# Performance work log

Measured on AMD Instinct MI355X. Metric: run time of the kernel, lower is better.

The kernel has to match this reference:

```python
import jax, jax.numpy as jnp
import numpy as np

E = 1024      # d_model
H = 16        # num heads
D = E // H    # head dim = 64
FF = 4096     # dim_feedforward
WIN = 128
EPS = 1e-5    # layer-norm eps
NEG = -1e9


def setup_inputs() -> dict:
    key = jax.random.key(0)
    ks = jax.random.split(key, 16)
    s = 0.02
    f32 = jnp.float32
    return {
        "src":       jax.random.normal(ks[0], (2, 2048, E), f32),
        "in_proj_w": jax.random.normal(ks[1], (3 * E, E), f32) * s,
        "in_proj_b": jnp.zeros((3 * E,), f32),
        "out_w":     jax.random.normal(ks[2], (E, E), f32) * s,
        "out_b":     jnp.zeros((E,), f32),
        "lin1_w":    jax.random.normal(ks[3], (FF, E), f32) * s,
        "lin1_b":    jnp.zeros((FF,), f32),
        "lin2_w":    jax.random.normal(ks[4], (E, FF), f32) * s,
        "lin2_b":    jnp.zeros((E,), f32),
        "ln1_g":     jnp.ones((E,), f32),
        "ln1_beta":  jnp.zeros((E,), f32),
        "ln2_g":     jnp.ones((E,), f32),
        "ln2_beta":  jnp.zeros((E,), f32),
    }


def _layer_norm(x, g, b):
    mu = x.mean(-1, keepdims=True)
    var = ((x - mu) ** 2).mean(-1, keepdims=True)
    return (x - mu) * jax.lax.rsqrt(var + EPS) * g + b


def reference(src, in_proj_w, in_proj_b, out_w, out_b,
              lin1_w, lin1_b, lin2_w, lin2_b,
              ln1_g, ln1_beta, ln2_g, ln2_beta):
    B, L, _ = src.shape  # batch_first=True
    x = src

    # fused QKV projection (torch Linear: y = x @ W.T + b)
    qkv = x @ in_proj_w.T + in_proj_b            # [B, L, 3E]
    q, k, v = jnp.split(qkv, 3, axis=-1)
    q = q.reshape(B, L, H, D)
    k = k.reshape(B, L, H, D)
    v = v.reshape(B, L, H, D)

    scores = jnp.einsum('blhd,bmhd->bhlm', q, k) / np.float32(np.sqrt(D))
    idx = jnp.arange(L)
    band = jnp.abs(idx[:, None] - idx[None, :]) <= WIN   # [L, L] allowed positions
    scores = jnp.where(band, scores, NEG)
    attn = jax.nn.softmax(scores, axis=-1)

    ctx = jnp.einsum('bhlm,bmhd->blhd', attn, v).reshape(B, L, E)
    attn_out = ctx @ out_w.T + out_b

    # post-norm transformer encoder layer (norm_first=False default)
    x = _layer_norm(x + attn_out, ln1_g, ln1_beta)
    ff = jax.nn.relu(x @ lin1_w.T + lin1_b) @ lin2_w.T + lin2_b
    return _layer_norm(x + ff, ln2_g, ln2_beta)
```

## Files before the change

### kernel.cpp

```cpp
#include <hip/hip_runtime.h>
#include <cstdint>
#include <cstddef>


typedef __attribute__((ext_vector_type(8))) short short8;
typedef __attribute__((ext_vector_type(4))) float f32x4;

__device__ __forceinline__ float b2f(unsigned short u) {
  union { unsigned int i; float f; } x; x.i = ((unsigned int)u) << 16; return x.f;
}
__device__ __forceinline__ unsigned short f2b(float f) {
  union { float f; unsigned int i; } x; x.f = f;
  unsigned int i = x.i;
  unsigned int r = (i + 0x7FFFu + ((i >> 16) & 1u)) >> 16;
  return (unsigned short)r;
}
__device__ __forceinline__ uint4 pack8(float4 f0, float4 f1) {
  uint4 r;
  r.x = (unsigned)f2b(f0.x) | ((unsigned)f2b(f0.y) << 16);
  r.y = (unsigned)f2b(f0.z) | ((unsigned)f2b(f0.w) << 16);
  r.z = (unsigned)f2b(f1.x) | ((unsigned)f2b(f1.y) << 16);
  r.w = (unsigned)f2b(f1.z) | ((unsigned)f2b(f1.w) << 16);
  return r;
}

__device__ __forceinline__ void gl_lds16(const unsigned short* g, unsigned short* l) {
  __builtin_amdgcn_global_load_lds(
      (const __attribute__((address_space(1))) unsigned int*)g,
      (__attribute__((address_space(3))) unsigned int*)l, 16, 0, 0);
}

__global__ __launch_bounds__(256) void conv3_k(
    const float* __restrict__ src, unsigned short* __restrict__ srcb,
    const float* __restrict__ w_in, const float* __restrict__ w_out,
    unsigned short* __restrict__ wslot)
{
  const int i = (blockIdx.x * 256 + threadIdx.x) * 8;
  const float* in;
  unsigned short* out;
  if (i < 4194304)      { in = src + i;                 out = srcb + i; }
  else if (i < 7340032) { in = w_in + (i - 4194304);    out = wslot + (i - 4194304); }
  else                  { in = w_out + (i - 7340032);   out = wslot + (i - 4194304); }
  const float4 f0 = *(const float4*)(in);
  const float4 f1 = *(const float4*)(in + 4);
  *(uint4*)(out) = pack8(f0, f1);
}

__global__ __launch_bounds__(256) void conv2_k(
    const float* __restrict__ w1, unsigned short* __restrict__ o1,
    const float* __restrict__ w2, unsigned short* __restrict__ o2)
{
  const int i = (blockIdx.x * 256 + threadIdx.x) * 8;
  const float* in;
  unsigned short* out;
  if (i < 4194304) { in = w1 + i;             out = o1 + i; }
  else             { in = w2 + (i - 4194304); out = o2 + (i - 4194304); }
  const float4 f0 = *(const float4*)(in);
  const float4 f1 = *(const float4*)(in + 4);
  *(uint4*)(out) = pack8(f0, f1);
}

template<int RELU, int OUT32>
__global__ __launch_bounds__(512, 2) void gemm256(
    const unsigned short* __restrict__ A, const unsigned short* __restrict__ Wb,
    const float* __restrict__ bias, void* __restrict__ out,
    int M, int N, int K)
{
  __shared__ unsigned short As[2][256 * 64];
  __shared__ unsigned short Bs[2][256 * 64];

  const int tid = threadIdx.x;
  const int lane = tid & 63, wid = tid >> 6;
  const int wm = wid >> 2, wn = wid & 3;

  const int gx = gridDim.x;
  const int flat = blockIdx.y * gx + blockIdx.x;
  const int chunk = (gx * gridDim.y) >> 3;
  const int nf = (flat & 7) * chunk + (flat >> 3);
  const int m0 = (nf / gx) * 256, n0 = (nf % gx) * 256;

  int offA[2][2], offB[2][2], ldsO2[2][2];
#pragma unroll
  for (int h1 = 0; h1 < 2; ++h1)
#pragma unroll
    for (int i = 0; i < 2; ++i) {
      const int sl = i * 512 + tid;
      const int r = h1 * 128 + (sl >> 3);
      const int sslot = sl & 7;
      const int c = (sslot + r) & 7;
      offA[h1][i] = (m0 + r) * K + c * 8;
      offB[h1][i] = (n0 + r) * K + c * 8;
      ldsO2[h1][i] = (h1 * 1024 + i * 512 + (tid & ~63)) * 8;
    }

  const int cl = lane & 15;
  const int kg = lane >> 4;

  int aoff[4][2], boff[2][2];
#pragma unroll
  for (int mt = 0; mt < 4; ++mt) {
    const int ar = wm * 64 + mt * 16 + cl;
#pragma unroll
    for (int ks = 0; ks < 2; ++ks)
      aoff[mt][ks] = ar * 64 + (((ks * 4 + kg) - ar) & 7) * 8;
  }
#pragma unroll
  for (int nt = 0; nt < 2; ++nt) {
    const int br = wn * 32 + nt * 16 + cl;
#pragma unroll
    for (int ks = 0; ks < 2; ++ks)
      boff[nt][ks] = br * 64 + (((ks * 4 + kg) - br) & 7) * 8;
  }

  f32x4 acc[8][4];
#pragma unroll
  for (int i = 0; i < 8; ++i)
#pragma unroll
    for (int j = 0; j < 4; ++j) acc[i][j] = (f32x4){0.f, 0.f, 0.f, 0.f};

  const int steps = K >> 6;

#define STAGE256(idx_) do { const int _x = (idx_); if (_x < 4 * steps) {        \
    const int T_ = _x >> 2, j_ = _x & 3, bf_ = T_ & 1; const int ko = T_ << 6;  \
    if (j_ == 0)      { gl_lds16(A  + offA[0][0] + ko, &As[bf_][ldsO2[0][0]]);  \
                        gl_lds16(A  + offA[0][1] + ko, &As[bf_][ldsO2[0][1]]); }\
    else if (j_ == 1) { gl_lds16(Wb + offB[0][0] + ko, &Bs[bf_][ldsO2[0][0]]);  \
                        gl_lds16(Wb + offB[0][1] + ko, &Bs[bf_][ldsO2[0][1]]); }\
    else if (j_ == 2) { gl_lds16(Wb + offB[1][0] + ko, &Bs[bf_][ldsO2[1][0]]);  \
                        gl_lds16(Wb + offB[1][1] + ko, &Bs[bf_][ldsO2[1][1]]); }\
    else              { gl_lds16(A  + offA[1][0] + ko, &As[bf_][ldsO2[1][0]]);  \
                        gl_lds16(A  + offA[1][1] + ko, &As[bf_][ldsO2[1][1]]); }\
  } } while (0)

  STAGE256(0); STAGE256(1); STAGE256(2); STAGE256(3);
  STAGE256(4); STAGE256(5); STAGE256(6);
  asm volatile("s_waitcnt vmcnt(6)" ::: "memory");
  __builtin_amdgcn_s_barrier();

  int cur = 0;
  for (int s = 0; s < steps; ++s) {
    short8 bf0[2][2], af[4][2];
#pragma unroll
    for (int nt = 0; nt < 2; ++nt)
#pragma unroll
      for (int ks = 0; ks < 2; ++ks) bf0[nt][ks] = *(const short8*)&Bs[cur][boff[nt][ks]];
#pragma unroll
    for (int mt = 0; mt < 4; ++mt)
#pragma unroll
      for (int ks = 0; ks < 2; ++ks) af[mt][ks] = *(const short8*)&As[cur][aoff[mt][ks]];
    STAGE256(4 * s + 7);
    asm volatile("s_waitcnt lgkmcnt(8)" ::: "memory");
    __builtin_amdgcn_s_barrier();
    asm volatile("s_waitcnt lgkmcnt(0)" ::: "memory");
    __builtin_amdgcn_sched_barrier(0);
    __builtin_amdgcn_s_setprio(1);
#pragma unroll
    for (int mt = 0; mt < 4; ++mt)
#pragma unroll
      for (int nt = 0; nt < 2; ++nt)
#pragma unroll
        for (int ks = 0; ks < 2; ++ks)
          acc[mt][nt] = __builtin_amdgcn_mfma_f32_16x16x32_bf16(af[mt][ks], bf0[nt][ks], acc[mt][nt], 0, 0, 0);
    __builtin_amdgcn_s_setprio(0);
    __builtin_amdgcn_s_barrier();

    short8 bf1[2][2];
#pragma unroll
    for (int nt = 0; nt < 2; ++nt)
#pragma unroll
      for (int ks = 0; ks < 2; ++ks) bf1[nt][ks] = *(const short8*)&Bs[cur][boff[nt][ks] + 8192];
    STAGE256(4 * s + 8);
    __builtin_amdgcn_s_barrier();
    asm volatile("s_waitcnt lgkmcnt(0)" ::: "memory");
    __builtin_amdgcn_sched_barrier(0);
    __builtin_amdgcn_s_setprio(1);
#pragma unroll
    for (int mt = 0; mt < 4; ++mt)
#pragma unroll
      for (int nt = 0; nt < 2; ++nt)
#pragma unroll
        for (int ks = 0; ks < 2; ++ks)
          acc[mt][nt + 2] = __builtin_amdgcn_mfma_f32_16x16x32_bf16(af[mt][ks], bf1[nt][ks], acc[mt][nt + 2], 0, 0, 0);
    __builtin_amdgcn_s_setprio(0);
    __builtin_amdgcn_s_barrier();

    short8 ag[4][2];
#pragma unroll
    for (int mt = 0; mt < 4; ++mt)
#pragma unroll
      for (int ks = 0; ks < 2; ++ks) ag[mt][ks] = *(const short8*)&As[cur][aoff[mt][ks] + 8192];
    STAGE256(4 * s + 9);
    __builtin_amdgcn_s_barrier();
    asm volatile("s_waitcnt lgkmcnt(0)" ::: "memory");
    __builtin_amdgcn_sched_barrier(0);
    __builtin_amdgcn_s_setprio(1);
#pragma unroll
    for (int mt = 0; mt < 4; ++mt)
#pragma unroll
      for (int nt = 0; nt < 2; ++nt)
#pragma unroll
        for (int ks = 0; ks < 2; ++ks)
          acc[mt + 4][nt] = __builtin_amdgcn_mfma_f32_16x16x32_bf16(ag[mt][ks], bf0[nt][ks], acc[mt + 4][nt], 0, 0, 0);
    __builtin_amdgcn_s_setprio(0);
    __builtin_amdgcn_s_barrier();

    STAGE256(4 * s + 10);
    if (s < steps - 2)       asm volatile("s_waitcnt vmcnt(6)" ::: "memory");
    else if (s == steps - 2) asm volatile("s_waitcnt vmcnt(0)" ::: "memory");
    __builtin_amdgcn_s_barrier();
    __builtin_amdgcn_s_setprio(1);
#pragma unroll
    for (int mt = 0; mt < 4; ++mt)
#pragma unroll
      for (int nt = 0; nt < 2; ++nt)
#pragma unroll
        for (int ks = 0; ks < 2; ++ks)
          acc[mt + 4][nt + 2] = __builtin_amdgcn_mfma_f32_16x16x32_bf16(ag[mt][ks], bf1[nt][ks], acc[mt + 4][nt + 2], 0, 0, 0);
    __builtin_amdgcn_s_setprio(0);
    __builtin_amdgcn_s_barrier();

    cur ^= 1;
  }
#undef STAGE256

#pragma unroll
  for (int nt = 0; nt < 4; ++nt) {
    const int colB = wn * 32 + (nt & 1) * 16 + (nt >> 1) * 128;
    const int col = n0 + colB + cl;
    const float bvs = bias[col];
#pragma unroll
    for (int mt = 0; mt < 8; ++mt) {
      const int rowA = wm * 64 + (mt & 3) * 16 + (mt >> 2) * 128;
#pragma unroll
      for (int r = 0; r < 4; ++r) {
        const int grow = m0 + rowA + kg * 4 + r;
        float v = acc[mt][nt][r] + bvs;
        if (RELU) v = fmaxf(v, 0.f);
        if (OUT32) ((float*)out)[(size_t)grow * N + col] = v;
        else       ((unsigned short*)out)[(size_t)grow * N + col] = f2b(v);
      }
    }
  }
}

template<int OUT32>
__global__ __launch_bounds__(256) void gemm64(
    const unsigned short* __restrict__ A, const unsigned short* __restrict__ Wb,
    const float* __restrict__ bias, void* __restrict__ out,
    int M, int N, int K)
{
  __shared__ unsigned short As[3][64 * 64];
  __shared__ unsigned short Bs[3][128 * 64];

  const int tid = threadIdx.x;
  const int lane = tid & 63, wid = tid >> 6;

  const int nwgx = gridDim.x;
  const int flat = blockIdx.y * nwgx + blockIdx.x;
  const int chunk = (nwgx * gridDim.y) >> 3;
  const int nf = (flat & 7) * chunk + (flat >> 3);
  const int m0 = (nf / nwgx) * 64, n0 = (nf % nwgx) * 128;

  const unsigned short* gA[2];
  const unsigned short* gW[4];
  int ldsA[2], ldsB[4];
#pragma unroll
  for (int i = 0; i < 2; ++i) {
    const int sl = wid * 128 + i * 64 + lane;
    const int r = sl >> 3, s = sl & 7, c = (s + r) & 7;
    gA[i] = A + (size_t)(m0 + r) * K + c * 8;
    ldsA[i] = (wid * 128 + i * 64) * 8;
  }
#pragma unroll
  for (int i = 0; i < 4; ++i) {
    const int sl = wid * 256 + i * 64 + lane;
    const int r = sl >> 3, s = sl & 7, c = (s + r) & 7;
    gW[i] = Wb + (size_t)(n0 + r) * K + c * 8;
    ldsB[i] = (wid * 256 + i * 64) * 8;
  }

  const int cl = lane & 15;
  const int kg = lane >> 4;
  int aoff[4][2], boff[2][2];
#pragma unroll
  for (int t = 0; t < 4; ++t) {
    const int ar = t * 16 + cl;
#pragma unroll
    for (int ks = 0; ks < 2; ++ks)
      aoff[t][ks] = ar * 64 + ((ks * 4 + kg - ar) & 7) * 8;
  }
#pragma unroll
  for (int t = 0; t < 2; ++t) {
    const int br = wid * 32 + t * 16 + cl;
#pragma unroll
    for (int ks = 0; ks < 2; ++ks)
      boff[t][ks] = br * 64 + ((ks * 4 + kg - br) & 7) * 8;
  }

  f32x4 acc[4][2];
#pragma unroll
  for (int i = 0; i < 4; ++i)
#pragma unroll
    for (int j = 0; j < 2; ++j) acc[i][j] = (f32x4){0.f, 0.f, 0.f, 0.f};

  const int steps = K >> 6;

  const int pre = steps < 3 ? steps : 3;
  for (int t = 0; t < pre; ++t) {
#pragma unroll
    for (int i = 0; i < 2; ++i) { gl_lds16(gA[i], &As[t][ldsA[i]]); gA[i] += 64; }
#pragma unroll
    for (int i = 0; i < 4; ++i) { gl_lds16(gW[i], &Bs[t][ldsB[i]]); gW[i] += 64; }
  }

  int cur = 0;
  for (int s = 0; s < steps; ++s) {
    const int rem = steps - 1 - s;
    if (rem >= 2)      asm volatile("s_waitcnt vmcnt(12)" ::: "memory");
    else if (rem == 1) asm volatile("s_waitcnt vmcnt(6)" ::: "memory");
    else               asm volatile("s_waitcnt vmcnt(0)" ::: "memory");
    __builtin_amdgcn_s_barrier();

    short8 af[4][2], bf[2][2];
#pragma unroll
    for (int t = 0; t < 4; ++t)
#pragma unroll
      for (int ks = 0; ks < 2; ++ks) af[t][ks] = *(const short8*)&As[cur][aoff[t][ks]];
#pragma unroll
    for (int t = 0; t < 2; ++t)
#pragma unroll
      for (int ks = 0; ks < 2; ++ks) bf[t][ks] = *(const short8*)&Bs[cur][boff[t][ks]];

    asm volatile("s_waitcnt lgkmcnt(0)" ::: "memory");
    __builtin_amdgcn_sched_barrier(0);
    __builtin_amdgcn_s_barrier();

    if (s + 3 < steps) {
#pragma unroll
      for (int i = 0; i < 2; ++i) { gl_lds16(gA[i], &As[cur][ldsA[i]]); gA[i] += 64; }
#pragma unroll
      for (int i = 0; i < 4; ++i) { gl_lds16(gW[i], &Bs[cur][ldsB[i]]); gW[i] += 64; }
    }

#pragma unroll
    for (int mt = 0; mt < 4; ++mt)
#pragma unroll
      for (int nt = 0; nt < 2; ++nt)
#pragma unroll
        for (int ks = 0; ks < 2; ++ks)
          acc[mt][nt] = __builtin_amdgcn_mfma_f32_16x16x32_bf16(af[mt][ks], bf[nt][ks], acc[mt][nt], 0, 0, 0);

    cur = (cur == 2) ? 0 : cur + 1;
  }

#pragma unroll
  for (int nt = 0; nt < 2; ++nt) {
    const int col = n0 + wid * 32 + nt * 16 + cl;
    const float bvs = bias[col];
#pragma unroll
    for (int mt = 0; mt < 4; ++mt) {
#pragma unroll
      for (int r = 0; r < 4; ++r) {
        const int grow = m0 + mt * 16 + kg * 4 + r;
        const float v = acc[mt][nt][r] + bvs;
        if (OUT32) ((float*)out)[(size_t)grow * N + col] = v;
        else       ((unsigned short*)out)[(size_t)grow * N + col] = f2b(v);
      }
    }
  }
}

__global__ __launch_bounds__(256) void attn_mfma(
    const unsigned short* __restrict__ qkv, unsigned short* __restrict__ ctx)
{
  __shared__ unsigned short Ks[64 * 72];
  __shared__ unsigned short Vt[64 * 72];
  __shared__ unsigned short Ps[64 * 72];

  const int tid = threadIdx.x;
  const int bid = blockIdx.x;
  const int qt = bid & 31, h = (bid >> 5) & 15, b = bid >> 9;
  const int q0 = qt * 64;
  const int wstart = max(0, q0 - 128);
  const int wend = min(2048, q0 + 64 + 128);
  const int ntile = (wend - wstart + 63) >> 6;
  const size_t rowb = (size_t)b * 2048;

  const int lane = tid & 63, wid = tid >> 6;
  const int cl = lane & 15;
  const int kq = (lane >> 4) * 8;
  const int rowg = lane >> 4;

  short8 aQ[2];
#pragma unroll
  for (int ks = 0; ks < 2; ++ks)
    aQ[ks] = *(const short8*)(qkv + (rowb + q0 + wid * 16 + cl) * 3072 + h * 64 + ks * 32 + kq);

  float m_i[4], l_i[4];
  f32x4 O[4];
#pragma unroll
  for (int r = 0; r < 4; ++r) { m_i[r] = -1.0e30f; l_i[r] = 0.f; }
#pragma unroll
  for (int nt = 0; nt < 4; ++nt) O[nt] = (f32x4){0.f, 0.f, 0.f, 0.f};

  for (int t = 0; t < ntile; ++t) {
    const int jbase = wstart + t * 64;
    __syncthreads();
    for (int idx = tid; idx < 512; idx += 256) {
      const int r = idx >> 3, c = idx & 7;
      const int jg = jbase + r;
      uint4 kv = {0u, 0u, 0u, 0u}, vv = {0u, 0u, 0u, 0u};
      if (jg < wend) {
        const size_t base = (rowb + jg) * 3072 + h * 64 + c * 8;
        kv = *(const uint4*)(qkv + base + 1024);
        vv = *(const uint4*)(qkv + base + 2048);
      }
      *(uint4*)&Ks[r * 72 + c * 8] = kv;
      const unsigned short* vs = (const unsigned short*)&vv;
#pragma unroll
      for (int ii = 0; ii < 8; ++ii) Vt[(c * 8 + ii) * 72 + r] = vs[ii];
    }
    __syncthreads();

    f32x4 S[4];
#pragma unroll
    for (int nt = 0; nt < 4; ++nt) S[nt] = (f32x4){0.f, 0.f, 0.f, 0.f};
#pragma unroll
    for (int nt = 0; nt < 4; ++nt)
#pragma unroll
      for (int ks = 0; ks < 2; ++ks) {
        const short8 bK = *(const short8*)&Ks[(nt * 16 + cl) * 72 + ks * 32 + kq];
        S[nt] = __builtin_amdgcn_mfma_f32_16x16x32_bf16(aQ[ks], bK, S[nt], 0, 0, 0);
      }

    float sc[4][4];
#pragma unroll
    for (int nt = 0; nt < 4; ++nt) {
      const int jg = jbase + nt * 16 + cl;
#pragma unroll
      for (int r = 0; r < 4; ++r) {
        const int i = q0 + wid * 16 + rowg * 4 + r;
        const bool v = (jg < wend) && (jg >= i - 128) && (jg <= i + 128);
        sc[nt][r] = v ? S[nt][r] * 0.125f : -1.0e30f;
      }
    }

    float alpha[4], p[4][4];
#pragma unroll
    for (int r = 0; r < 4; ++r) {
      float tm = fmaxf(fmaxf(sc[0][r], sc[1][r]), fmaxf(sc[2][r], sc[3][r]));
      tm = fmaxf(tm, __shfl_xor(tm, 1, 64));
      tm = fmaxf(tm, __shfl_xor(tm, 2, 64));
      tm = fmaxf(tm, __shfl_xor(tm, 4, 64));
      tm = fmaxf(tm, __shfl_xor(tm, 8, 64));
      const float mn = fmaxf(m_i[r], tm);
      alpha[r] = __expf(m_i[r] - mn);
      m_i[r] = mn;
      float ps = 0.f;
#pragma unroll
      for (int nt = 0; nt < 4; ++nt) { p[nt][r] = __expf(sc[nt][r] - mn); ps += p[nt][r]; }
      ps += __shfl_xor(ps, 1, 64);
      ps += __shfl_xor(ps, 2, 64);
      ps += __shfl_xor(ps, 4, 64);
      ps += __shfl_xor(ps, 8, 64);
      l_i[r] = l_i[r] * alpha[r] + ps;
    }

#pragma unroll
    for (int nt = 0; nt < 4; ++nt)
#pragma unroll
      for (int r = 0; r < 4; ++r)
        Ps[(wid * 16 + rowg * 4 + r) * 72 + nt * 16 + cl] = f2b(p[nt][r]);
    __syncthreads();

#pragma unroll
    for (int nt = 0; nt < 4; ++nt)
#pragma unroll
      for (int r = 0; r < 4; ++r) O[nt][r] *= alpha[r];
    short8 aP[2];
#pragma unroll
    for (int ks = 0; ks < 2; ++ks)
      aP[ks] = *(const short8*)&Ps[(wid * 16 + cl) * 72 + ks * 32 + kq];
#pragma unroll
    for (int nt = 0; nt < 4; ++nt)
#pragma unroll
      for (int ks = 0; ks < 2; ++ks) {
        const short8 bV = *(const short8*)&Vt[(nt * 16 + cl) * 72 + ks * 32 + kq];
        O[nt] = __builtin_amdgcn_mfma_f32_16x16x32_bf16(aP[ks], bV, O[nt], 0, 0, 0);
      }
  }

#pragma unroll
  for (int nt = 0; nt < 4; ++nt) {
    const int d = nt * 16 + cl;
#pragma unroll
    for (int r = 0; r < 4; ++r) {
      const int i = q0 + wid * 16 + rowg * 4 + r;
      ctx[(rowb + i) * 1024 + h * 64 + d] = f2b(O[nt][r] / l_i[r]);
    }
  }
}

template<int AF32, int BF32, int OF32>
__global__ __launch_bounds__(256) void ln_k(
    const void* __restrict__ a, const void* __restrict__ b,
    const float* __restrict__ g, const float* __restrict__ be,
    void* __restrict__ o)
{
  __shared__ float rbuf[8];
  const int tid = threadIdx.x;
  const size_t base = (size_t)blockIdx.x * 1024;
  const int lane = tid & 63, wid = tid >> 6;
  const int c0 = tid * 4;

  float av[4], bv[4], xv[4];
  if (AF32) {
    const float4 t = *(const float4*)((const float*)a + base + c0);
    av[0] = t.x; av[1] = t.y; av[2] = t.z; av[3] = t.w;
  } else {
    const uint2 t = *(const uint2*)((const unsigned short*)a + base + c0);
    av[0] = b2f((unsigned short)(t.x & 0xffffu)); av[1] = b2f((unsigned short)(t.x >> 16));
    av[2] = b2f((unsigned short)(t.y & 0xffffu)); av[3] = b2f((unsigned short)(t.y >> 16));
  }
  if (BF32) {
    const float4 t = *(const float4*)((const float*)b + base + c0);
    bv[0] = t.x; bv[1] = t.y; bv[2] = t.z; bv[3] = t.w;
  } else {
    const uint2 t = *(const uint2*)((const unsigned short*)b + base + c0);
    bv[0] = b2f((unsigned short)(t.x & 0xffffu)); bv[1] = b2f((unsigned short)(t.x >> 16));
    bv[2] = b2f((unsigned short)(t.y & 0xffffu)); bv[3] = b2f((unsigned short)(t.y >> 16));
  }

  float s = 0.f, sq = 0.f;
#pragma unroll
  for (int t = 0; t < 4; ++t) {
    const float x = av[t] + bv[t];
    xv[t] = x; s += x; sq += x * x;
  }
  for (int o2 = 1; o2 < 64; o2 <<= 1) { s += __shfl_xor(s, o2, 64); sq += __shfl_xor(sq, o2, 64); }
  if (lane == 0) { rbuf[wid] = s; rbuf[wid + 4] = sq; }
  __syncthreads();
  s  = rbuf[0] + rbuf[1] + rbuf[2] + rbuf[3];
  sq = rbuf[4] + rbuf[5] + rbuf[6] + rbuf[7];
  const float mean = s * (1.0f / 1024.f);
  const float var = sq * (1.0f / 1024.f) - mean * mean;
  const float rstd = rsqrtf(var + 1e-5f);

  const float4 gv  = *(const float4*)(g + c0);
  const float4 bev = *(const float4*)(be + c0);
  float y[4];
  y[0] = (xv[0] - mean) * rstd * gv.x + bev.x;
  y[1] = (xv[1] - mean) * rstd * gv.y + bev.y;
  y[2] = (xv[2] - mean) * rstd * gv.z + bev.z;
  y[3] = (xv[3] - mean) * rstd * gv.w + bev.w;

  if (OF32) {
    float4 t; t.x = y[0]; t.y = y[1]; t.z = y[2]; t.w = y[3];
    *(float4*)((float*)o + base + c0) = t;
  } else {
    uint2 t;
    t.x = (unsigned)f2b(y[0]) | ((unsigned)f2b(y[1]) << 16);
    t.y = (unsigned)f2b(y[2]) | ((unsigned)f2b(y[3]) << 16);
    *(uint2*)((unsigned short*)o + base + c0) = t;
  }
}

extern "C" void kernel_launch(void* const* d_in, const int* in_sizes, int n_in,
                              void* d_out, int out_size, void* d_ws, size_t ws_size,
                              hipStream_t stream)
{
  (void)in_sizes; (void)n_in; (void)out_size; (void)ws_size;
  const float* src   = (const float*)d_in[0];
  const float* w_in  = (const float*)d_in[1];
  const float* b_in  = (const float*)d_in[2];
  const float* w_out = (const float*)d_in[3];
  const float* b_out = (const float*)d_in[4];
  const float* w1    = (const float*)d_in[5];
  const float* b1    = (const float*)d_in[6];
  const float* w2    = (const float*)d_in[7];
  const float* b2    = (const float*)d_in[8];
  const float* g1    = (const float*)d_in[9];
  const float* be1   = (const float*)d_in[10];
  const float* g2    = (const float*)d_in[11];
  const float* be2   = (const float*)d_in[12];

  char* ws = (char*)d_ws;
  unsigned short* srcb  = (unsigned short*)(ws);
  unsigned short* x1b   = srcb;
  unsigned short* qkv   = (unsigned short*)(ws + 8388608);
  unsigned short* ctx   = (unsigned short*)(ws + 33554432);
  unsigned short* attnb = (unsigned short*)(ws + 8388608);
  unsigned short* ff1   = (unsigned short*)(ws + 8388608);
  unsigned short* wslot = (unsigned short*)(ws + 41943040);
  float*          outf  = (float*)d_out;
  unsigned short* w2b   = (unsigned short*)d_out;

  conv3_k<<<dim3(4096), 256, 0, stream>>>(src, srcb, w_in, w_out, wslot);
  gemm256<0, 0><<<dim3(12, 16), 512, 0, stream>>>(srcb, wslot, b_in, qkv, 4096, 3072, 1024);
  attn_mfma<<<dim3(1024), 256, 0, stream>>>(qkv, ctx);
  gemm64<0><<<dim3(8, 64), 256, 0, stream>>>(ctx, wslot + 3145728, b_out, attnb, 4096, 1024, 1024);
  ln_k<0, 0, 0><<<dim3(4096), 256, 0, stream>>>(srcb, attnb, g1, be1, x1b);
  conv2_k<<<dim3(4096), 256, 0, stream>>>(w1, wslot, w2, w2b);
  gemm256<1, 0><<<dim3(16, 16), 512, 0, stream>>>(x1b, wslot, b1, ff1, 4096, 4096, 1024);
  gemm64<0><<<dim3(8, 64), 256, 0, stream>>>(ff1, w2b, b2, wslot, 4096, 1024, 4096);
  ln_k<0, 0, 1><<<dim3(4096), 256, 0, stream>>>(x1b, wslot, g2, be2, outf);
}
```

Before: 299.6 us.

## Replace 4-wave 64x128 GEMM with single-wave 64x64 tile kernel

The N=1024 GEMMs (out-proj and FFN down-proj) now use a single-wavefront workgroup computing a 64x64 tile, with double buffering in place of triple buffering. Because only one wave touches shared memory, the workgroup barriers go away, and the grid grows to 1024 workgroups so the GPU is better filled. The cost is that each workgroup loads its own A tile without sharing it across waves, which roughly doubles global/LDS traffic per flop. Each wave now holds a 4x4 accumulator tile, which raises register pressure. With only two buffers there is less prefetch depth to hide latency.

```diff
diff --git a/kernel.cpp b/kernel.cpp
--- a/kernel.cpp
+++ b/kernel.cpp
@@ -244,118 +244,99 @@
 }
 
 template<int OUT32>
-__global__ __launch_bounds__(256) void gemm64(
+__global__ __launch_bounds__(64) void gemm64w(
     const unsigned short* __restrict__ A, const unsigned short* __restrict__ Wb,
     const float* __restrict__ bias, void* __restrict__ out,
     int M, int N, int K)
 {
-  __shared__ unsigned short As[3][64 * 64];
-  __shared__ unsigned short Bs[3][128 * 64];
-
-  const int tid = threadIdx.x;
-  const int lane = tid & 63, wid = tid >> 6;
-
-  const int nwgx = gridDim.x;
-  const int flat = blockIdx.y * nwgx + blockIdx.x;
-  const int chunk = (nwgx * gridDim.y) >> 3;
+  __shared__ unsigned short As[2][64 * 64];
+  __shared__ unsigned short Bs[2][64 * 64];
+
+  const int lane = threadIdx.x;
+
+  const int gx = gridDim.x;
+  const int flat = blockIdx.y * gx + blockIdx.x;
+  const int chunk = (gx * gridDim.y) >> 3;
   const int nf = (flat & 7) * chunk + (flat >> 3);
-  const int m0 = (nf / nwgx) * 64, n0 = (nf % nwgx) * 128;
-
-  const unsigned short* gA[2];
-  const unsigned short* gW[4];
-  int ldsA[2], ldsB[4];
-#pragma unroll
-  for (int i = 0; i < 2; ++i) {
-    const int sl = wid * 128 + i * 64 + lane;
+  const int m0 = (nf / gx) * 64, n0 = (nf % gx) * 64;
+
+  int offA[8], offB[8], ldsO[8];
+#pragma unroll
+  for (int i = 0; i < 8; ++i) {
+    const int sl = i * 64 + lane;
     const int r = sl >> 3, s = sl & 7, c = (s + r) & 7;
-    gA[i] = A + (size_t)(m0 + r) * K + c * 8;
-    ldsA[i] = (wid * 128 + i * 64) * 8;
-  }
-#pragma unroll
-  for (int i = 0; i < 4; ++i) {
-    const int sl = wid * 256 + i * 64 + lane;
-    const int r = sl >> 3, s = sl & 7, c = (s + r) & 7;
-    gW[i] = Wb + (size_t)(n0 + r) * K + c * 8;
-    ldsB[i] = (wid * 256 + i * 64) * 8;
+    offA[i] = (m0 + r) * K + c * 8;
+    offB[i] = (n0 + r) * K + c * 8;
+    ldsO[i] = i * 512;
   }
 
   const int cl = lane & 15;
   const int kg = lane >> 4;
-  int aoff[4][2], boff[2][2];
+  int aoff[4][2], boff[4][2];
 #pragma unroll
   for (int t = 0; t < 4; ++t) {
-    const int ar = t * 16 + cl;
-#pragma unroll
-    for (int ks = 0; ks < 2; ++ks)
-      aoff[t][ks] = ar * 64 + ((ks * 4 + kg - ar) & 7) * 8;
-  }
-#pragma unroll
-  for (int t = 0; t < 2; ++t) {
-    const int br = wid * 32 + t * 16 + cl;
-#pragma unroll
-    for (int ks = 0; ks < 2; ++ks)
-      boff[t][ks] = br * 64 + ((ks * 4 + kg - br) & 7) * 8;
-  }
-
-  f32x4 acc[4][2];
+    const int rr = t * 16 + cl;
+#pragma unroll
+    for (int ks = 0; ks < 2; ++ks) {
+      aoff[t][ks] = rr * 64 + ((ks * 4 + kg - rr) & 7) * 8;
+      boff[t][ks] = rr * 64 + ((ks * 4 + kg - rr) & 7) * 8;
+    }
+  }
+
+  f32x4 acc[4][4];
 #pragma unroll
   for (int i = 0; i < 4; ++i)
 #pragma unroll
-    for (int j = 0; j < 2; ++j) acc[i][j] = (f32x4){0.f, 0.f, 0.f, 0.f};
+    for (int j = 0; j < 4; ++j) acc[i][j] = (f32x4){0.f, 0.f, 0.f, 0.f};
 
   const int steps = K >> 6;
 
-  const int pre = steps < 3 ? steps : 3;
+  const int pre = steps < 2 ? steps : 2;
   for (int t = 0; t < pre; ++t) {
-#pragma unroll
-    for (int i = 0; i < 2; ++i) { gl_lds16(gA[i], &As[t][ldsA[i]]); gA[i] += 64; }
-#pragma unroll
-    for (int i = 0; i < 4; ++i) { gl_lds16(gW[i], &Bs[t][ldsB[i]]); gW[i] += 64; }
-  }
-
-  int cur = 0;
+    const int ko = t * 64;
+#pragma unroll
+    for (int i = 0; i < 8; ++i) gl_lds16(A + offA[i] + ko, &As[t][ldsO[i]]);
+#pragma unroll
+    for (int i = 0; i < 8; ++i) gl_lds16(Wb + offB[i] + ko, &Bs[t][ldsO[i]]);
+  }
+
   for (int s = 0; s < steps; ++s) {
-    const int rem = steps - 1 - s;
-    if (rem >= 2)      asm volatile("s_waitcnt vmcnt(12)" ::: "memory");
-    else if (rem == 1) asm volatile("s_waitcnt vmcnt(6)" ::: "memory");
+    const int cur = s & 1;
+    if (s + 1 < steps) asm volatile("s_waitcnt vmcnt(16)" ::: "memory");
     else               asm volatile("s_waitcnt vmcnt(0)" ::: "memory");
-    __builtin_amdgcn_s_barrier();
-
-    short8 af[4][2], bf[2][2];
+
+    short8 af[4][2], bf[4][2];
 #pragma unroll
     for (int t = 0; t < 4; ++t)
 #pragma unroll
-      for (int ks = 0; ks < 2; ++ks) af[t][ks] = *(const short8*)&As[cur][aoff[t][ks]];
-#pragma unroll
-    for (int t = 0; t < 2; ++t)
-#pragma unroll
-      for (int ks = 0; ks < 2; ++ks) bf[t][ks] = *(const short8*)&Bs[cur][boff[t][ks]];
+      for (int ks = 0; ks < 2; ++ks) {
+        af[t][ks] = *(const short8*)&As[cur][aoff[t][ks]];
+        bf[t][ks] = *(const short8*)&Bs[cur][boff[t][ks]];
+      }
 
     asm volatile("s_waitcnt lgkmcnt(0)" ::: "memory");
     __builtin_amdgcn_sched_barrier(0);
-    __builtin_amdgcn_s_barrier();
-
-    if (s + 3 < steps) {
-#pragma unroll
-      for (int i = 0; i < 2; ++i) { gl_lds16(gA[i], &As[cur][ldsA[i]]); gA[i] += 64; }
-#pragma unroll
-      for (int i = 0; i < 4; ++i) { gl_lds16(gW[i], &Bs[cur][ldsB[i]]); gW[i] += 64; }
-    }
-
-#pragma unroll
-    for (int mt = 0; mt < 4; ++mt)
-#pragma unroll
-      for (int nt = 0; nt < 2; ++nt)
+
+    if (s + 2 < steps) {
+      const int ko = (s + 2) * 64;
+#pragma unroll
+      for (int i = 0; i < 8; ++i) gl_lds16(A + offA[i] + ko, &As[cur][ldsO[i]]);
+#pragma unroll
+      for (int i = 0; i < 8; ++i) gl_lds16(Wb + offB[i] + ko, &Bs[cur][ldsO[i]]);
+    }
+
+#pragma unroll
+    for (int mt = 0; mt < 4; ++mt)
+#pragma unroll
+      for (int nt = 0; nt < 4; ++nt)
 #pragma unroll
         for (int ks = 0; ks < 2; ++ks)
           acc[mt][nt] = __builtin_amdgcn_mfma_f32_16x16x32_bf16(af[mt][ks], bf[nt][ks], acc[mt][nt], 0, 0, 0);
-
-    cur = (cur == 2) ? 0 : cur + 1;
-  }
-
-#pragma unroll
-  for (int nt = 0; nt < 2; ++nt) {
-    const int col = n0 + wid * 32 + nt * 16 + cl;
+  }
+
+#pragma unroll
+  for (int nt = 0; nt < 4; ++nt) {
+    const int col = n0 + nt * 16 + cl;
     const float bvs = bias[col];
 #pragma unroll
     for (int mt = 0; mt < 4; ++mt) {
@@ -598,10 +579,10 @@
   conv3_k<<<dim3(4096), 256, 0, stream>>>(src, srcb, w_in, w_out, wslot);
   gemm256<0, 0><<<dim3(12, 16), 512, 0, stream>>>(srcb, wslot, b_in, qkv, 4096, 3072, 1024);
   attn_mfma<<<dim3(1024), 256, 0, stream>>>(qkv, ctx);
-  gemm64<0><<<dim3(8, 64), 256, 0, stream>>>(ctx, wslot + 3145728, b_out, attnb, 4096, 1024, 1024);
+  gemm64w<0><<<dim3(16, 64), 64, 0, stream>>>(ctx, wslot + 3145728, b_out, attnb, 4096, 1024, 1024);
   ln_k<0, 0, 0><<<dim3(4096), 256, 0, stream>>>(srcb, attnb, g1, be1, x1b);
   conv2_k<<<dim3(4096), 256, 0, stream>>>(w1, wslot, w2, w2b);
   gemm256<1, 0><<<dim3(16, 16), 512, 0, stream>>>(x1b, wslot, b1, ff1, 4096, 4096, 1024);
-  gemm64<0><<<dim3(8, 64), 256, 0, stream>>>(ff1, w2b, b2, wslot, 4096, 1024, 4096);
+  gemm64w<0><<<dim3(16, 64), 64, 0, stream>>>(ff1, w2b, b2, wslot, 4096, 1024, 4096);
   ln_k<0, 0, 1><<<dim3(4096), 256, 0, stream>>>(x1b, wslot, g2, be2, outf);
 }
```

New measurement: 300.6 us. No clear change (+0.3%).

## Load K tiles via direct global-to-LDS with swizzled layouts in banded attention

Applied to the files above, without the earlier changes.

The attention kernel now loads K tiles with direct global-to-LDS copies (gl_lds16) into an unpadded, rotation-swizzled buffer. V is transposed into LDS using an XOR swizzle, and all global and LDS addresses are precomputed outside the tile loop. The tile-count rounding and the jg<wend bounds check are dropped because window lengths are always multiples of 64. The goal is to cut register staging, bank conflicts and address arithmetic in the attention kernel. This relies on the fixed sequence length and window sizes.

```diff
diff --git a/kernel.cpp b/kernel.cpp
--- a/kernel.cpp
+++ b/kernel.cpp
@@ -373,7 +373,7 @@
 __global__ __launch_bounds__(256) void attn_mfma(
     const unsigned short* __restrict__ qkv, unsigned short* __restrict__ ctx)
 {
-  __shared__ unsigned short Ks[64 * 72];
+  __shared__ unsigned short Ks[64 * 64];
   __shared__ unsigned short Vt[64 * 72];
   __shared__ unsigned short Ps[64 * 72];
 
@@ -383,13 +383,43 @@
   const int q0 = qt * 64;
   const int wstart = max(0, q0 - 128);
   const int wend = min(2048, q0 + 64 + 128);
-  const int ntile = (wend - wstart + 63) >> 6;
+  const int ntile = (wend - wstart) >> 6;
   const size_t rowb = (size_t)b * 2048;
 
   const int lane = tid & 63, wid = tid >> 6;
   const int cl = lane & 15;
-  const int kq = (lane >> 4) * 8;
-  const int rowg = lane >> 4;
+  const int kg = lane >> 4;
+  const int kq = kg * 8;
+  const int rowg = kg;
+
+  const unsigned short* gK[2];
+  int ldsK[2];
+#pragma unroll
+  for (int i = 0; i < 2; ++i) {
+    const int sl = i * 256 + tid;
+    const int r = sl >> 3, s = sl & 7, c = (s + r) & 7;
+    gK[i] = qkv + (rowb + wstart + r) * 3072 + h * 64 + 1024 + c * 8;
+    ldsK[i] = (i * 256 + (tid & ~63)) * 8;
+  }
+  const unsigned short* gV[2];
+  int vr[2], vc[2];
+#pragma unroll
+  for (int i = 0; i < 2; ++i) {
+    const int idx = i * 256 + tid;
+    vr[i] = idx >> 3; vc[i] = idx & 7;
+    gV[i] = qkv + (rowb + wstart + vr[i]) * 3072 + h * 64 + 2048 + vc[i] * 8;
+  }
+
+  int koff[4][2], voff[4][2];
+#pragma unroll
+  for (int nt = 0; nt < 4; ++nt) {
+    const int jr = nt * 16 + cl;
+#pragma unroll
+    for (int ks = 0; ks < 2; ++ks) {
+      koff[nt][ks] = jr * 64 + (((ks * 4 + kg) - jr) & 7) * 8;
+      voff[nt][ks] = jr * 72 + ((ks * 32 + kq) ^ (((jr >> 3) & 7) << 3));
+    }
+  }
 
   short8 aQ[2];
 #pragma unroll
@@ -406,19 +436,23 @@
   for (int t = 0; t < ntile; ++t) {
     const int jbase = wstart + t * 64;
     __syncthreads();
-    for (int idx = tid; idx < 512; idx += 256) {
-      const int r = idx >> 3, c = idx & 7;
-      const int jg = jbase + r;
-      uint4 kv = {0u, 0u, 0u, 0u}, vv = {0u, 0u, 0u, 0u};
-      if (jg < wend) {
-        const size_t base = (rowb + jg) * 3072 + h * 64 + c * 8;
-        kv = *(const uint4*)(qkv + base + 1024);
-        vv = *(const uint4*)(qkv + base + 2048);
-      }
-      *(uint4*)&Ks[r * 72 + c * 8] = kv;
-      const unsigned short* vs = (const unsigned short*)&vv;
-#pragma unroll
-      for (int ii = 0; ii < 8; ++ii) Vt[(c * 8 + ii) * 72 + r] = vs[ii];
+    gl_lds16(gK[0], &Ks[ldsK[0]]);
+    gl_lds16(gK[1], &Ks[ldsK[1]]);
+    gK[0] += 196608; gK[1] += 196608;
+    const uint4 v0 = *(const uint4*)gV[0];
+    const uint4 v1 = *(const uint4*)gV[1];
+    gV[0] += 196608; gV[1] += 196608;
+    {
+      const unsigned short* p = (const unsigned short*)&v0;
+      const int col = vr[0] ^ (vc[0] << 3);
+#pragma unroll
+      for (int ii = 0; ii < 8; ++ii) Vt[(vc[0] * 8 + ii) * 72 + col] = p[ii];
+    }
+    {
+      const unsigned short* p = (const unsigned short*)&v1;
+      const int col = vr[1] ^ (vc[1] << 3);
+#pragma unroll
+      for (int ii = 0; ii < 8; ++ii) Vt[(vc[1] * 8 + ii) * 72 + col] = p[ii];
     }
     __syncthreads();
 
@@ -429,7 +463,7 @@
     for (int nt = 0; nt < 4; ++nt)
 #pragma unroll
       for (int ks = 0; ks < 2; ++ks) {
-        const short8 bK = *(const short8*)&Ks[(nt * 16 + cl) * 72 + ks * 32 + kq];
+        const short8 bK = *(const short8*)&Ks[koff[nt][ks]];
         S[nt] = __builtin_amdgcn_mfma_f32_16x16x32_bf16(aQ[ks], bK, S[nt], 0, 0, 0);
       }
 
@@ -440,7 +474,7 @@
 #pragma unroll
       for (int r = 0; r < 4; ++r) {
         const int i = q0 + wid * 16 + rowg * 4 + r;
-        const bool v = (jg < wend) && (jg >= i - 128) && (jg <= i + 128);
+        const bool v = (jg >= i - 128) && (jg <= i + 128);
         sc[nt][r] = v ? S[nt][r] * 0.125f : -1.0e30f;
       }
     }
@@ -485,7 +519,7 @@
     for (int nt = 0; nt < 4; ++nt)
 #pragma unroll
       for (int ks = 0; ks < 2; ++ks) {
-        const short8 bV = *(const short8*)&Vt[(nt * 16 + cl) * 72 + ks * 32 + kq];
+        const short8 bV = *(const short8*)&Vt[voff[nt][ks]];
         O[nt] = __builtin_amdgcn_mfma_f32_16x16x32_bf16(aP[ks], bV, O[nt], 0, 0, 0);
       }
   }
```

Measured after the change: 295.8 us. About the same (-1.3%).
